# Performance work log

Hardware: AMD Instinct MI355X
Metric: run time of the kernel (lower is better)

## Reference

```python
import jax, jax.numpy as jnp
import numpy as np

FEATURE_DIM = 512


def setup_inputs() -> dict:
    key = jax.random.key(0)
    ks = jax.random.split(key, 12)
    B, Nv, Dv = 32, 1024, 768
    Nl, Dl = 77, 512
    D = FEATURE_DIM
    s = lambda fan_in: 1.0 / np.sqrt(fan_in)
    return {
        "fv": jax.random.normal(ks[0], (B, Nv, Dv), jnp.float32),
        "fl": jax.random.normal(ks[1], (B, Nl, Dl), jnp.float32),
        # linear_vk / linear_vv: Dv -> D (stored as [in, out])
        "W_vk": jax.random.uniform(ks[2], (Dv, D), jnp.float32, -s(Dv), s(Dv)),
        "b_vk": jax.random.uniform(ks[3], (D,), jnp.float32, -s(Dv), s(Dv)),
        "W_vv": jax.random.uniform(ks[4], (Dv, D), jnp.float32, -s(Dv), s(Dv)),
        "b_vv": jax.random.uniform(ks[5], (D,), jnp.float32, -s(Dv), s(Dv)),
        # linear_lk / linear_lv: Dl -> D
        "W_lk": jax.random.uniform(ks[6], (Dl, D), jnp.float32, -s(Dl), s(Dl)),
        "b_lk": jax.random.uniform(ks[7], (D,), jnp.float32, -s(Dl), s(Dl)),
        "W_lv": jax.random.uniform(ks[8], (Dl, D), jnp.float32, -s(Dl), s(Dl)),
        "b_lv": jax.random.uniform(ks[9], (D,), jnp.float32, -s(Dl), s(Dl)),
        # linear_m: nl(77) -> 768
        "W_m": jax.random.uniform(ks[10], (Nl, 768), jnp.float32, -s(Nl), s(Nl)),
        "b_m": jax.random.uniform(ks[11], (768,), jnp.float32, -s(Nl), s(Nl)),
    }


def reference(fv, fl, W_vk, b_vk, W_vv, b_vv, W_lk, b_lk, W_lv, b_lv, W_m, b_m):
    # projections
    fk_v = jnp.einsum("bvd,de->bve", fv, W_vk) + b_vk   # [B, Nv, D]
    fv_v = jnp.einsum("bvd,de->bve", fv, W_vv) + b_vv   # [B, Nv, D]
    fk_l = jnp.einsum("bld,de->ble", fl, W_lk) + b_lk   # [B, Nl, D]
    fv_l = jnp.einsum("bld,de->ble", fl, W_lv) + b_lv   # [B, Nl, D]
    # shared score matrix [B, Nl, Nv]
    a_raw = jnp.einsum("ble,bve->blv", fk_l, fk_v) / jnp.sqrt(
        jnp.asarray(FEATURE_DIM, fk_l.dtype))
    # dual softmax: over Nv for language queries, over Nl for vision queries
    fa_v = jnp.einsum("blv,bve->ble", jax.nn.softmax(a_raw, axis=-1), fv_v)  # [B, Nl, D]
    fa_l = jnp.einsum("bvl,ble->bve",
                      jax.nn.softmax(jnp.swapaxes(a_raw, -1, -2), axis=-1),
                      fv_l)                                                  # [B, Nv, D]
    # fm = fa_v @ fa_l^T -> [B, Nl, Nv]; transpose(1,2) -> [B, Nv, Nl]
    fm = jnp.einsum("bve,ble->bvl", fa_l, fa_v)          # [B, Nv, Nl]
    return jnp.einsum("bvl,lo->bvo", fm, W_m) + b_m      # [B, Nv, 768]
```

## Files before the change

kernel.cpp:

```cpp
#include <hip/hip_runtime.h>


using s16x8  = __attribute__((ext_vector_type(8))) short;
using f32x4v = __attribute__((ext_vector_type(4))) float;

__device__ __forceinline__ unsigned short f2bf(float f) {
  unsigned int u = __float_as_uint(f);
  u += 0x7fffu + ((u >> 16) & 1u);
  return (unsigned short)(u >> 16);
}
__device__ __forceinline__ float bf2f(unsigned short h) {
  return __uint_as_float(((unsigned int)h) << 16);
}
__device__ __forceinline__ void split2(float v, unsigned short &hh, unsigned short &ll) {
  hh = f2bf(v);
  ll = f2bf(v - bf2f(hh));
}
__device__ __forceinline__ void split8v(float4 a, float4 b, s16x8& H, s16x8& L) {
  unsigned short hh, ll;
  split2(a.x, hh, ll); H[0] = (short)hh; L[0] = (short)ll;
  split2(a.y, hh, ll); H[1] = (short)hh; L[1] = (short)ll;
  split2(a.z, hh, ll); H[2] = (short)hh; L[2] = (short)ll;
  split2(a.w, hh, ll); H[3] = (short)hh; L[3] = (short)ll;
  split2(b.x, hh, ll); H[4] = (short)hh; L[4] = (short)ll;
  split2(b.y, hh, ll); H[5] = (short)hh; L[5] = (short)ll;
  split2(b.z, hh, ll); H[6] = (short)hh; L[6] = (short)ll;
  split2(b.w, hh, ll); H[7] = (short)hh; L[7] = (short)ll;
}

__device__ __forceinline__ void gload16(const unsigned short* g, unsigned short* l) {
  __builtin_amdgcn_global_load_lds(
      (const __attribute__((address_space(1))) unsigned int*)(const void*)g,
      (__attribute__((address_space(3))) unsigned int*)(void*)l,
      16, 0, 0);
}

__global__ __launch_bounds__(256) void prep_weight(const float* __restrict__ W,
                                                   unsigned short* __restrict__ Wh,
                                                   unsigned short* __restrict__ Wl,
                                                   int K, int N, int Kpad) {
  __shared__ float tile[32][33];
  int nb = blockIdx.x * 32, kb = blockIdx.y * 32;
  int tx = threadIdx.x & 31, ty = threadIdx.x >> 5;
  #pragma unroll
  for (int i = 0; i < 32; i += 8) {
    int k = kb + ty + i, n = nb + tx;
    tile[ty + i][tx] = (k < K && n < N) ? W[(long)k * N + n] : 0.f;
  }
  __syncthreads();
  #pragma unroll
  for (int i = 0; i < 32; i += 8) {
    int n = nb + ty + i, k = kb + tx;
    if (n < N && k < Kpad) {
      unsigned short hh, ll;
      split2(tile[tx][ty + i], hh, ll);
      Wh[(long)n * Kpad + k] = hh;
      Wl[(long)n * Kpad + k] = ll;
    }
  }
}

struct GemmArgs {
  const unsigned short *Ah, *Alo, *Bh, *Blo;
  const float *Af;
  int K;
  int Mld, Nld;
  int lda, ldb;
  long long sA, sB;
};

template <bool AF32, bool SWZ, int NJ, class Epi>
__global__ __launch_bounds__(256, 4) void gemm3(GemmArgs g, Epi epi) {
  constexpr int BN  = NJ * 32;
  constexpr int ASZ = 128 * 32;
  constexpr int BSZ = BN * 32;
  __shared__ __align__(16) unsigned short sm[2 * ASZ + 2 * BSZ];
  unsigned short* sAh = sm;
  unsigned short* sAl = sm + ASZ;
  unsigned short* sBh = sm + 2 * ASZ;
  unsigned short* sBl = sm + 2 * ASZ + BSZ;

  int bidx = blockIdx.x, bidy = blockIdx.y;
  if constexpr (SWZ) {
    int nx = gridDim.x;
    int nwg = nx * gridDim.y;
    int orig = bidx + bidy * nx;
    int swz = (orig & 7) * (nwg >> 3) + (orig >> 3);
    bidx = swz % nx; bidy = swz / nx;
  }

  const int t    = threadIdx.x;
  const int b    = blockIdx.z;
  const int m0   = bidy * 128;
  const int n0   = bidx * BN;
  const int lane = t & 63;
  const int w    = t >> 6;
  const int wr   = (w >> 1) * 64;
  const int wc   = (w & 1) * (NJ * 16);

  const long long aBase = (long long)b * g.sA;
  const long long bBase = (long long)b * g.sB;

  const int clk = lane & 3;
  const int rwB = (NJ == 4) ? ((w << 5) + (lane >> 2)) : ((w << 4) + (lane >> 2));
  const int sckB = ((clk ^ ((rwB >> 1) & 3)) << 3);
  int br0 = n0 + rwB;      if (br0 > g.Nld - 1) br0 = g.Nld - 1;
  int br1 = n0 + rwB + 16; if (br1 > g.Nld - 1) br1 = g.Nld - 1;
  const long long bR0d = bBase + (long long)br0 * g.ldb + sckB;
  const long long bR1d = bBase + (long long)br1 * g.ldb + sckB;
  const int dB0 = (NJ == 4) ? (w << 10) : (w << 9);
  const int dB1 = dB0 + 512;
  const int rwA = (w << 5) + (lane >> 2);
  const int sckA = ((clk ^ ((rwA >> 1) & 3)) << 3);
  int arD0 = m0 + rwA;      if (arD0 > g.Mld - 1) arD0 = g.Mld - 1;
  int arD1 = m0 + rwA + 16; if (arD1 > g.Mld - 1) arD1 = g.Mld - 1;
  const long long aR0d = aBase + (long long)arD0 * g.lda + sckA;
  const long long aR1d = aBase + (long long)arD1 * g.lda + sckA;
  const int dA0 = w << 10, dA1 = (w << 10) + 512;

  const int rA0 = t >> 2, rA1 = 64 + (t >> 2), cc = t & 3;
  const int cOff = cc << 3;
  int mr0 = m0 + rA0; if (mr0 > g.Mld - 1) mr0 = g.Mld - 1;
  int mr1 = m0 + rA1; if (mr1 > g.Mld - 1) mr1 = g.Mld - 1;
  const long long aR0 = aBase + (long long)mr0 * g.lda;
  const long long aR1 = aBase + (long long)mr1 * g.lda;
  const int wA0 = rA0 * 32 + ((cc ^ ((rA0 >> 1) & 3)) << 3);
  const int wA1 = rA1 * 32 + ((cc ^ ((rA1 >> 1) & 3)) << 3);

  int roffA[4], roffB[NJ];
  #pragma unroll
  for (int i = 0; i < 4; ++i) {
    int row = wr + i * 16 + (lane & 15);
    int ch  = lane >> 4;
    roffA[i] = row * 32 + ((ch ^ ((row >> 1) & 3)) << 3);
  }
  #pragma unroll
  for (int j = 0; j < NJ; ++j) {
    int row = wc + j * 16 + (lane & 15);
    int ch  = lane >> 4;
    roffB[j] = row * 32 + ((ch ^ ((row >> 1) & 3)) << 3);
  }

  f32x4v acc[4][NJ];
  #pragma unroll
  for (int i = 0; i < 4; ++i)
    #pragma unroll
    for (int j = 0; j < NJ; ++j)
      #pragma unroll
      for (int r = 0; r < 4; ++r) acc[i][j][r] = 0.f;

  float4 pa0, pa1, pa2, pa3;

  auto issueDMA = [&](int k0) {
    gload16(g.Bh  + (bR0d + k0), sBh + dB0);
    gload16(g.Blo + (bR0d + k0), sBl + dB0);
    if constexpr (NJ == 4) {
      gload16(g.Bh  + (bR1d + k0), sBh + dB1);
      gload16(g.Blo + (bR1d + k0), sBl + dB1);
    }
    if constexpr (!AF32) {
      gload16(g.Ah  + (aR0d + k0), sAh + dA0);
      gload16(g.Ah  + (aR1d + k0), sAh + dA1);
      gload16(g.Alo + (aR0d + k0), sAl + dA0);
      gload16(g.Alo + (aR1d + k0), sAl + dA1);
    }
  };
  auto issueA = [&](int k0) {
    if constexpr (AF32) {
      const float* s0 = g.Af + (aR0 + k0 + cOff);
      const float* s1 = g.Af + (aR1 + k0 + cOff);
      pa0 = *(const float4*)s0; pa1 = *(const float4*)(s0 + 4);
      pa2 = *(const float4*)s1; pa3 = *(const float4*)(s1 + 4);
    }
  };
  auto writeA = [&]() {
    if constexpr (AF32) {
      s16x8 H, L;
      split8v(pa0, pa1, H, L);
      *(s16x8*)(sAh + wA0) = H; *(s16x8*)(sAl + wA0) = L;
      split8v(pa2, pa3, H, L);
      *(s16x8*)(sAh + wA1) = H; *(s16x8*)(sAl + wA1) = L;
    }
  };

  issueDMA(0);
  if constexpr (AF32) { issueA(0); writeA(); }
  const int nkt = g.K >> 5;
  for (int kt = 0; kt < nkt; ++kt) {
    asm volatile("s_waitcnt vmcnt(0)" ::: "memory");
    __syncthreads();
    if (AF32 && kt + 1 < nkt) issueA((kt + 1) << 5);
    s16x8 ah[4], al[4], bh[NJ], bl[NJ];
    #pragma unroll
    for (int i = 0; i < 4; ++i) {
      ah[i] = *(const s16x8*)(sAh + roffA[i]);
      al[i] = *(const s16x8*)(sAl + roffA[i]);
    }
    #pragma unroll
    for (int j = 0; j < NJ; ++j) {
      bh[j] = *(const s16x8*)(sBh + roffB[j]);
      bl[j] = *(const s16x8*)(sBl + roffB[j]);
    }
    #pragma unroll
    for (int i = 0; i < 4; ++i)
      #pragma unroll
      for (int j = 0; j < NJ; ++j) {
        acc[i][j] = __builtin_amdgcn_mfma_f32_16x16x32_bf16(ah[i], bh[j], acc[i][j], 0, 0, 0);
        acc[i][j] = __builtin_amdgcn_mfma_f32_16x16x32_bf16(ah[i], bl[j], acc[i][j], 0, 0, 0);
        acc[i][j] = __builtin_amdgcn_mfma_f32_16x16x32_bf16(al[i], bh[j], acc[i][j], 0, 0, 0);
      }
    __syncthreads();
    if (kt + 1 < nkt) {
      writeA();
      issueDMA((kt + 1) << 5);
    }
  }
  #pragma unroll
  for (int i = 0; i < 4; ++i)
    #pragma unroll
    for (int j = 0; j < NJ; ++j) {
      int mm = m0 + wr + i * 16 + ((lane >> 4) << 2);
      int nn = n0 + wc + j * 16 + (lane & 15);
      epi(b, mm, nn, acc[i][j]);
    }
}

struct EpiBF16Pair {
  unsigned short *h, *lo; const float* bias; long long bs; int ld; int Mst;
  __device__ void operator()(int b, int m, int n, f32x4v v) const {
    float bb = bias ? bias[n] : 0.f;
    #pragma unroll
    for (int r = 0; r < 4; ++r) {
      int mm = m + r;
      if (mm < Mst) {
        long long o = (long long)b * bs + (long long)mm * ld + n;
        unsigned short hh, ll;
        split2(v[r] + bb, hh, ll);
        h[o] = hh; lo[o] = ll;
      }
    }
  }
};

struct EpiDualL {
  unsigned short *kh, *kl, *vh, *vl; const float *bk, *bv;
  __device__ void operator()(int, int m, int n, f32x4v v) const {
    bool lo512 = n < 512;
    float bb = lo512 ? bk[n] : bv[n - 512];
    int nn = lo512 ? n : n - 512;
    unsigned short* H = lo512 ? kh : vh;
    unsigned short* L = lo512 ? kl : vl;
    #pragma unroll
    for (int r = 0; r < 4; ++r) {
      int mm = m + r;
      if (mm < 2464) {
        long long o = (long long)mm * 512 + nn;
        unsigned short hh, ll;
        split2(v[r] + bb, hh, ll);
        H[o] = hh; L[o] = ll;
      }
    }
  }
};

struct EpiDualV {
  unsigned short *kh, *kl, *vh, *vl; const float *bk, *bv;
  __device__ void operator()(int, int m, int n, f32x4v v) const {
    if (n < 512) {
      float bb = bk[n];
      #pragma unroll
      for (int r = 0; r < 4; ++r) {
        long long o = (long long)(m + r) * 512 + n;
        unsigned short hh, ll;
        split2(v[r] + bb, hh, ll);
        kh[o] = hh; kl[o] = ll;
      }
    } else {
      int b2 = m >> 10, vv = m & 1023;
      float bb = bv[n - 512];
      ushort4 H, L;
      split2(v[0] + bb, H.x, L.x); split2(v[1] + bb, H.y, L.y);
      split2(v[2] + bb, H.z, L.z); split2(v[3] + bb, H.w, L.w);
      long long o = ((long long)b2 * 512 + (n - 512)) * 1024 + vv;
      *(ushort4*)(vh + o) = H;
      *(ushort4*)(vl + o) = L;
    }
  }
};

struct EpiScore {
  float* out;
  __device__ void operator()(int b, int m, int n, f32x4v v) const {
    #pragma unroll
    for (int r = 0; r < 4; ++r) {
      int mm = m + r;
      if (mm < 77)
        out[((long long)b * 77 + mm) * 1024 + n] = v[r] * 0.04419417382415922f;
    }
  }
};

struct EpiTransT {
  unsigned short *h, *lo;
  __device__ void operator()(int b, int m, int n, f32x4v v) const {
    #pragma unroll
    for (int r = 0; r < 4; ++r) {
      int mm = m + r;
      float val = (mm < 77) ? v[r] : 0.f;
      long long o = (long long)b * 98304 + (long long)n * 128 + mm;
      unsigned short hh, ll;
      split2(val, hh, ll);
      h[o] = hh; lo[o] = ll;
    }
  }
};

struct EpiOutB {
  float* out; const float* bias;
  __device__ void operator()(int b, int m, int n, f32x4v v) const {
    float bb = bias[n];
    #pragma unroll
    for (int r = 0; r < 4; ++r)
      out[(long long)(b * 1024 + m + r) * 768 + n] = v[r] + bb;
  }
};

__global__ __launch_bounds__(256) void softmax_rows(const float* __restrict__ a,
                                                    unsigned short* __restrict__ Ph,
                                                    unsigned short* __restrict__ Plo) {
  long row = blockIdx.x;
  const float* src = a + row * 1024;
  int t = threadIdx.x;
  float4 x = ((const float4*)src)[t];
  float mx = fmaxf(fmaxf(x.x, x.y), fmaxf(x.z, x.w));
  #pragma unroll
  for (int o = 32; o; o >>= 1) mx = fmaxf(mx, __shfl_xor(mx, o));
  __shared__ float red[4], red2[4];
  int w = t >> 6;
  if ((t & 63) == 0) red[w] = mx;
  __syncthreads();
  mx = fmaxf(fmaxf(red[0], red[1]), fmaxf(red[2], red[3]));
  float e0 = __expf(x.x - mx), e1 = __expf(x.y - mx);
  float e2 = __expf(x.z - mx), e3 = __expf(x.w - mx);
  float s = e0 + e1 + e2 + e3;
  #pragma unroll
  for (int o = 32; o; o >>= 1) s += __shfl_xor(s, o);
  if ((t & 63) == 0) red2[w] = s;
  __syncthreads();
  s = red2[0] + red2[1] + red2[2] + red2[3];
  float inv = 1.f / s;
  ushort4 H, L;
  split2(e0 * inv, H.x, L.x); split2(e1 * inv, H.y, L.y);
  split2(e2 * inv, H.z, L.z); split2(e3 * inv, H.w, L.w);
  long o = row * 1024 + (long)t * 4;
  *(ushort4*)(Ph + o)  = H;
  *(ushort4*)(Plo + o) = L;
}

__global__ __launch_bounds__(128) void softmax_cols(const float* __restrict__ a,
                                                    unsigned short* __restrict__ Ph,
                                                    unsigned short* __restrict__ Plo) {
  __shared__ float tile[77 * 129];
  __shared__ float inv[128];
  int t = threadIdx.x;
  int c = blockIdx.x;
  int b = blockIdx.y;
  const float* src = a + (long)b * 77 * 1024 + c * 128;
  for (int r = 0; r < 77; ++r) tile[r * 129 + t] = src[(long)r * 1024 + t];
  __syncthreads();
  float mx = -1e30f;
  for (int r = 0; r < 77; ++r) mx = fmaxf(mx, tile[r * 129 + t]);
  float s = 0.f;
  for (int r = 0; r < 77; ++r) {
    float e = __expf(tile[r * 129 + t] - mx);
    tile[r * 129 + t] = e;
    s += e;
  }
  inv[t] = 1.f / s;
  __syncthreads();
  unsigned short* dh = Ph  + ((long)b * 1024 + c * 128) * 128;
  unsigned short* dl = Plo + ((long)b * 1024 + c * 128) * 128;
  for (int vb = 0; vb < 128; vb += 2) {
    int v = vb + (t >> 6);
    int k = (t & 63) * 2;
    float iv = inv[v];
    float p0 = (k     < 77) ? tile[k * 129 + v] * iv       : 0.f;
    float p1 = (k + 1 < 77) ? tile[(k + 1) * 129 + v] * iv : 0.f;
    ushort2 H, L;
    split2(p0, H.x, L.x); split2(p1, H.y, L.y);
    *(ushort2*)(dh + (long)v * 128 + k) = H;
    *(ushort2*)(dl + (long)v * 128 + k) = L;
  }
}

extern "C" void kernel_launch(void* const* d_in, const int* in_sizes, int n_in,
                              void* d_out, int out_size, void* d_ws, size_t ws_size,
                              hipStream_t stream) {
  const float* fv   = (const float*)d_in[0];
  const float* fl   = (const float*)d_in[1];
  const float* W_vk = (const float*)d_in[2];
  const float* b_vk = (const float*)d_in[3];
  const float* W_vv = (const float*)d_in[4];
  const float* b_vv = (const float*)d_in[5];
  const float* W_lk = (const float*)d_in[6];
  const float* b_lk = (const float*)d_in[7];
  const float* W_lv = (const float*)d_in[8];
  const float* b_lv = (const float*)d_in[9];
  const float* W_m  = (const float*)d_in[10];
  const float* b_m  = (const float*)d_in[11];

  char* base = (char*)d_ws;
  size_t off = 0;
  auto take = [&](size_t bytes) -> char* {
    char* p = base + off;
    off = (off + bytes + 255) & ~(size_t)255;
    return p;
  };

  unsigned short* wcatv_h = (unsigned short*)take(1572864);
  unsigned short* wcatv_l = (unsigned short*)take(1572864);
  unsigned short* wcatl_h = (unsigned short*)take(1048576);
  unsigned short* wcatl_l = (unsigned short*)take(1048576);
  unsigned short* wm_h    = (unsigned short*)take(196608);
  unsigned short* wm_l    = (unsigned short*)take(196608);
  unsigned short* fkl_h  = (unsigned short*)take(2523136);
  unsigned short* fkl_l  = (unsigned short*)take(2523136);
  unsigned short* fvl_h  = (unsigned short*)take(2523136);
  unsigned short* fvl_l  = (unsigned short*)take(2523136);
  unsigned short* fkv_h  = (unsigned short*)take(33554432);
  unsigned short* fkv_l  = (unsigned short*)take(33554432);
  unsigned short* fvvT_h = (unsigned short*)take(33554432);
  unsigned short* fvvT_l = (unsigned short*)take(33554432);
  float*          araw   = (float*)take(10092544);
  unsigned short* p1_h   = (unsigned short*)take(5046272);
  unsigned short* p1_l   = (unsigned short*)take(5046272);
  unsigned short* p2t_h  = (unsigned short*)take(8388608);
  unsigned short* p2t_l  = (unsigned short*)take(8388608);
  unsigned short* fav_h  = (unsigned short*)take(4194304);
  unsigned short* fav_l  = (unsigned short*)take(4194304);
  unsigned short* s_h    = (unsigned short*)take(1048576);
  unsigned short* s_l    = (unsigned short*)take(1048576);
  unsigned short* tt_h   = (unsigned short*)take(6291456);
  unsigned short* tt_l   = (unsigned short*)take(6291456);

  if (off > ws_size) return;

  prep_weight<<<dim3(16, 24), 256, 0, stream>>>(W_vk, wcatv_h, wcatv_l, 768, 512, 768);
  prep_weight<<<dim3(16, 24), 256, 0, stream>>>(W_vv, wcatv_h + 512 * 768, wcatv_l + 512 * 768, 768, 512, 768);
  prep_weight<<<dim3(16, 16), 256, 0, stream>>>(W_lk, wcatl_h, wcatl_l, 512, 512, 512);
  prep_weight<<<dim3(16, 16), 256, 0, stream>>>(W_lv, wcatl_h + 512 * 512, wcatl_l + 512 * 512, 512, 512, 512);
  prep_weight<<<dim3(24, 4), 256, 0, stream>>>(W_m, wm_h, wm_l, 77, 768, 128);

  {
    GemmArgs g{}; g.Af = fl; g.Bh = wcatl_h; g.Blo = wcatl_l;
    g.K = 512; g.Mld = 2464; g.Nld = 1024; g.lda = 512; g.ldb = 512; g.sA = 0; g.sB = 0;
    EpiDualL e{fkl_h, fkl_l, fvl_h, fvl_l, b_lk, b_lv};
    gemm3<true, false, 4, EpiDualL><<<dim3(8, 20, 1), 256, 0, stream>>>(g, e);
  }
  {
    GemmArgs g{}; g.Af = fv; g.Bh = wcatv_h; g.Blo = wcatv_l;
    g.K = 768; g.Mld = 32768; g.Nld = 1024; g.lda = 768; g.ldb = 768; g.sA = 0; g.sB = 0;
    EpiDualV e{fkv_h, fkv_l, fvvT_h, fvvT_l, b_vk, b_vv};
    gemm3<true, true, 4, EpiDualV><<<dim3(8, 256, 1), 256, 0, stream>>>(g, e);
  }
  {
    GemmArgs g{}; g.Ah = fkl_h; g.Alo = fkl_l; g.Bh = fkv_h; g.Blo = fkv_l;
    g.K = 512; g.Mld = 77; g.Nld = 1024; g.lda = 512; g.ldb = 512;
    g.sA = 77 * 512; g.sB = 1024 * 512;
    EpiScore e{araw};
    gemm3<false, false, 2, EpiScore><<<dim3(16, 1, 32), 256, 0, stream>>>(g, e);
  }
  softmax_rows<<<2464, 256, 0, stream>>>(araw, p1_h, p1_l);
  softmax_cols<<<dim3(8, 32), 128, 0, stream>>>(araw, p2t_h, p2t_l);
  {
    GemmArgs g{}; g.Ah = p1_h; g.Alo = p1_l; g.Bh = fvvT_h; g.Blo = fvvT_l;
    g.K = 1024; g.Mld = 77; g.Nld = 512; g.lda = 1024; g.ldb = 1024;
    g.sA = 77 * 1024; g.sB = 512 * 1024;
    EpiBF16Pair e{fav_h, fav_l, nullptr, 128 * 512, 512, 128};
    gemm3<false, false, 2, EpiBF16Pair><<<dim3(8, 1, 32), 256, 0, stream>>>(g, e);
  }
  {
    GemmArgs g{}; g.Ah = fvl_h; g.Alo = fvl_l; g.Bh = fav_h; g.Blo = fav_l;
    g.K = 512; g.Mld = 77; g.Nld = 128; g.lda = 512; g.ldb = 512;
    g.sA = 77 * 512; g.sB = 128 * 512;
    EpiBF16Pair e{s_h, s_l, nullptr, 128 * 128, 128, 128};
    gemm3<false, false, 2, EpiBF16Pair><<<dim3(2, 1, 32), 256, 0, stream>>>(g, e);
  }
  {
    GemmArgs g{}; g.Ah = s_h; g.Alo = s_l; g.Bh = wm_h; g.Blo = wm_l;
    g.K = 128; g.Mld = 128; g.Nld = 768; g.lda = 128; g.ldb = 128;
    g.sA = 128 * 128; g.sB = 0;
    EpiTransT e{tt_h, tt_l};
    gemm3<false, false, 2, EpiTransT><<<dim3(12, 1, 32), 256, 0, stream>>>(g, e);
  }
  {
    GemmArgs g{}; g.Ah = p2t_h; g.Alo = p2t_l; g.Bh = tt_h; g.Blo = tt_l;
    g.K = 128; g.Mld = 1024; g.Nld = 768; g.lda = 128; g.ldb = 128;
    g.sA = 1024 * 128; g.sB = 768 * 128;
    EpiOutB e{(float*)d_out, b_m};
    gemm3<false, false, 4, EpiOutB><<<dim3(6, 8, 32), 256, 0, stream>>>(g, e);
  }
  (void)in_sizes; (void)n_in; (void)out_size;
}
```

Baseline: 650.3 us.

## Double-buffer GEMM LDS tiles, add MI tile param, merge weight prep launches

Replaces the single-buffered GEMM with a ping-pong LDS pipeline. Loads for the next k-tile are issued into the alternate buffer before computing the current one, and the second barrier per iteration is removed. Adds an MI template parameter so the small batched GEMMs use 64-row tiles with twice as many blocks, and merges the five weight-prep launches into one kernel. The cost is doubled LDS per block, with launch bounds lowered to 2 blocks per CU, which may reduce occupancy.

```diff
diff --git a/kernel.cpp b/kernel.cpp
--- a/kernel.cpp
+++ b/kernel.cpp
@@ -35,27 +35,34 @@
       16, 0, 0);
 }
 
-__global__ __launch_bounds__(256) void prep_weight(const float* __restrict__ W,
-                                                   unsigned short* __restrict__ Wh,
-                                                   unsigned short* __restrict__ Wl,
-                                                   int K, int N, int Kpad) {
+struct PrepSeg { const float* W; unsigned short* Wh; unsigned short* Wl;
+                 int K, N, Kpad, ntx, tOff; };
+struct PrepArgs { PrepSeg s[5]; };
+
+__global__ __launch_bounds__(256) void prep_all(PrepArgs pa) {
   __shared__ float tile[32][33];
-  int nb = blockIdx.x * 32, kb = blockIdx.y * 32;
+  int bid = blockIdx.x;
+  int si = 0;
+  #pragma unroll
+  for (int i = 1; i < 5; ++i) if (bid >= pa.s[i].tOff) si = i;
+  PrepSeg sg = pa.s[si];
+  int local = bid - sg.tOff;
+  int nb = (local % sg.ntx) * 32, kb = (local / sg.ntx) * 32;
   int tx = threadIdx.x & 31, ty = threadIdx.x >> 5;
   #pragma unroll
   for (int i = 0; i < 32; i += 8) {
     int k = kb + ty + i, n = nb + tx;
-    tile[ty + i][tx] = (k < K && n < N) ? W[(long)k * N + n] : 0.f;
+    tile[ty + i][tx] = (k < sg.K && n < sg.N) ? sg.W[(long)k * sg.N + n] : 0.f;
   }
   __syncthreads();
   #pragma unroll
   for (int i = 0; i < 32; i += 8) {
     int n = nb + ty + i, k = kb + tx;
-    if (n < N && k < Kpad) {
+    if (n < sg.N && k < sg.Kpad) {
       unsigned short hh, ll;
       split2(tile[tx][ty + i], hh, ll);
-      Wh[(long)n * Kpad + k] = hh;
-      Wl[(long)n * Kpad + k] = ll;
+      sg.Wh[(long)n * sg.Kpad + k] = hh;
+      sg.Wl[(long)n * sg.Kpad + k] = ll;
     }
   }
 }
@@ -69,16 +76,13 @@
   long long sA, sB;
 };
 
-template <bool AF32, bool SWZ, int NJ, class Epi>
-__global__ __launch_bounds__(256, 4) void gemm3(GemmArgs g, Epi epi) {
-  constexpr int BN  = NJ * 32;
-  constexpr int ASZ = 128 * 32;
-  constexpr int BSZ = BN * 32;
-  __shared__ __align__(16) unsigned short sm[2 * ASZ + 2 * BSZ];
-  unsigned short* sAh = sm;
-  unsigned short* sAl = sm + ASZ;
-  unsigned short* sBh = sm + 2 * ASZ;
-  unsigned short* sBl = sm + 2 * ASZ + BSZ;
+template <bool AF32, bool SWZ, int MI, int NJ, class Epi>
+__global__ __launch_bounds__(256, 2) void gemmP(GemmArgs g, Epi epi) {
+  static_assert(!AF32 || MI == 4, "AF32 path assumes MI==4");
+  constexpr int ASZ = MI * 1024;
+  constexpr int BSZ = NJ * 1024;
+  constexpr int BUF = 2 * ASZ + 2 * BSZ;
+  __shared__ __align__(16) unsigned short sm[2 * BUF];
 
   int bidx = blockIdx.x, bidy = blockIdx.y;
   if constexpr (SWZ) {
@@ -91,11 +95,11 @@
 
   const int t    = threadIdx.x;
   const int b    = blockIdx.z;
-  const int m0   = bidy * 128;
-  const int n0   = bidx * BN;
+  const int m0   = bidy * (MI * 32);
+  const int n0   = bidx * (NJ * 32);
   const int lane = t & 63;
   const int w    = t >> 6;
-  const int wr   = (w >> 1) * 64;
+  const int wr   = (w >> 1) * (MI * 16);
   const int wc   = (w & 1) * (NJ * 16);
 
   const long long aBase = (long long)b * g.sA;
@@ -108,15 +112,16 @@
   int br1 = n0 + rwB + 16; if (br1 > g.Nld - 1) br1 = g.Nld - 1;
   const long long bR0d = bBase + (long long)br0 * g.ldb + sckB;
   const long long bR1d = bBase + (long long)br1 * g.ldb + sckB;
-  const int dB0 = (NJ == 4) ? (w << 10) : (w << 9);
+  const int dB0 = w * ((NJ == 4) ? 1024 : 512);
   const int dB1 = dB0 + 512;
-  const int rwA = (w << 5) + (lane >> 2);
+  const int rwA = (MI == 4) ? ((w << 5) + (lane >> 2)) : ((w << 4) + (lane >> 2));
   const int sckA = ((clk ^ ((rwA >> 1) & 3)) << 3);
   int arD0 = m0 + rwA;      if (arD0 > g.Mld - 1) arD0 = g.Mld - 1;
   int arD1 = m0 + rwA + 16; if (arD1 > g.Mld - 1) arD1 = g.Mld - 1;
   const long long aR0d = aBase + (long long)arD0 * g.lda + sckA;
   const long long aR1d = aBase + (long long)arD1 * g.lda + sckA;
-  const int dA0 = w << 10, dA1 = (w << 10) + 512;
+  const int dA0 = w * ((MI == 4) ? 1024 : 512);
+  const int dA1 = dA0 + 512;
 
   const int rA0 = t >> 2, rA1 = 64 + (t >> 2), cc = t & 3;
   const int cOff = cc << 3;
@@ -127,9 +132,9 @@
   const int wA0 = rA0 * 32 + ((cc ^ ((rA0 >> 1) & 3)) << 3);
   const int wA1 = rA1 * 32 + ((cc ^ ((rA1 >> 1) & 3)) << 3);
 
-  int roffA[4], roffB[NJ];
-  #pragma unroll
-  for (int i = 0; i < 4; ++i) {
+  int roffA[MI], roffB[NJ];
+  #pragma unroll
+  for (int i = 0; i < MI; ++i) {
     int row = wr + i * 16 + (lane & 15);
     int ch  = lane >> 4;
     roffA[i] = row * 32 + ((ch ^ ((row >> 1) & 3)) << 3);
@@ -141,9 +146,9 @@
     roffB[j] = row * 32 + ((ch ^ ((row >> 1) & 3)) << 3);
   }
 
-  f32x4v acc[4][NJ];
-  #pragma unroll
-  for (int i = 0; i < 4; ++i)
+  f32x4v acc[MI][NJ];
+  #pragma unroll
+  for (int i = 0; i < MI; ++i)
     #pragma unroll
     for (int j = 0; j < NJ; ++j)
       #pragma unroll
@@ -151,18 +156,21 @@
 
   float4 pa0, pa1, pa2, pa3;
 
-  auto issueDMA = [&](int k0) {
-    gload16(g.Bh  + (bR0d + k0), sBh + dB0);
-    gload16(g.Blo + (bR0d + k0), sBl + dB0);
+  auto issueDMA = [&](int k0, int p) {
+    unsigned short* bb = sm + p * BUF;
+    gload16(g.Bh  + (bR0d + k0), bb + 2 * ASZ + dB0);
+    gload16(g.Blo + (bR0d + k0), bb + 2 * ASZ + BSZ + dB0);
     if constexpr (NJ == 4) {
-      gload16(g.Bh  + (bR1d + k0), sBh + dB1);
-      gload16(g.Blo + (bR1d + k0), sBl + dB1);
+      gload16(g.Bh  + (bR1d + k0), bb + 2 * ASZ + dB1);
+      gload16(g.Blo + (bR1d + k0), bb + 2 * ASZ + BSZ + dB1);
     }
     if constexpr (!AF32) {
-      gload16(g.Ah  + (aR0d + k0), sAh + dA0);
-      gload16(g.Ah  + (aR1d + k0), sAh + dA1);
-      gload16(g.Alo + (aR0d + k0), sAl + dA0);
-      gload16(g.Alo + (aR1d + k0), sAl + dA1);
+      gload16(g.Ah  + (aR0d + k0), bb + dA0);
+      gload16(g.Alo + (aR0d + k0), bb + ASZ + dA0);
+      if constexpr (MI == 4) {
+        gload16(g.Ah  + (aR1d + k0), bb + dA1);
+        gload16(g.Alo + (aR1d + k0), bb + ASZ + dA1);
+      }
     }
   };
   auto issueA = [&](int k0) {
@@ -173,50 +181,53 @@
       pa2 = *(const float4*)s1; pa3 = *(const float4*)(s1 + 4);
     }
   };
-  auto writeA = [&]() {
+  auto writeA = [&](int p) {
     if constexpr (AF32) {
+      unsigned short* base = sm + p * BUF;
       s16x8 H, L;
       split8v(pa0, pa1, H, L);
-      *(s16x8*)(sAh + wA0) = H; *(s16x8*)(sAl + wA0) = L;
+      *(s16x8*)(base + wA0) = H; *(s16x8*)(base + ASZ + wA0) = L;
       split8v(pa2, pa3, H, L);
-      *(s16x8*)(sAh + wA1) = H; *(s16x8*)(sAl + wA1) = L;
+      *(s16x8*)(base + wA1) = H; *(s16x8*)(base + ASZ + wA1) = L;
     }
   };
 
-  issueDMA(0);
-  if constexpr (AF32) { issueA(0); writeA(); }
+  issueDMA(0, 0);
+  if constexpr (AF32) { issueA(0); writeA(0); }
+  int p = 0;
   const int nkt = g.K >> 5;
   for (int kt = 0; kt < nkt; ++kt) {
     asm volatile("s_waitcnt vmcnt(0)" ::: "memory");
     __syncthreads();
-    if (AF32 && kt + 1 < nkt) issueA((kt + 1) << 5);
-    s16x8 ah[4], al[4], bh[NJ], bl[NJ];
-    #pragma unroll
-    for (int i = 0; i < 4; ++i) {
-      ah[i] = *(const s16x8*)(sAh + roffA[i]);
-      al[i] = *(const s16x8*)(sAl + roffA[i]);
+    if (kt + 1 < nkt) {
+      issueDMA((kt + 1) << 5, p ^ 1);
+      issueA((kt + 1) << 5);
+    }
+    unsigned short* base = sm + p * BUF;
+    s16x8 ah[MI], al[MI], bh[NJ], bl[NJ];
+    #pragma unroll
+    for (int i = 0; i < MI; ++i) {
+      ah[i] = *(const s16x8*)(base + roffA[i]);
+      al[i] = *(const s16x8*)(base + ASZ + roffA[i]);
     }
     #pragma unroll
     for (int j = 0; j < NJ; ++j) {
-      bh[j] = *(const s16x8*)(sBh + roffB[j]);
-      bl[j] = *(const s16x8*)(sBl + roffB[j]);
-    }
-    #pragma unroll
-    for (int i = 0; i < 4; ++i)
+      bh[j] = *(const s16x8*)(base + 2 * ASZ + roffB[j]);
+      bl[j] = *(const s16x8*)(base + 2 * ASZ + BSZ + roffB[j]);
+    }
+    #pragma unroll
+    for (int i = 0; i < MI; ++i)
       #pragma unroll
       for (int j = 0; j < NJ; ++j) {
         acc[i][j] = __builtin_amdgcn_mfma_f32_16x16x32_bf16(ah[i], bh[j], acc[i][j], 0, 0, 0);
         acc[i][j] = __builtin_amdgcn_mfma_f32_16x16x32_bf16(ah[i], bl[j], acc[i][j], 0, 0, 0);
         acc[i][j] = __builtin_amdgcn_mfma_f32_16x16x32_bf16(al[i], bh[j], acc[i][j], 0, 0, 0);
       }
-    __syncthreads();
-    if (kt + 1 < nkt) {
-      writeA();
-      issueDMA((kt + 1) << 5);
-    }
-  }
-  #pragma unroll
-  for (int i = 0; i < 4; ++i)
+    if (kt + 1 < nkt) writeA(p ^ 1);
+    p ^= 1;
+  }
+  #pragma unroll
+  for (int i = 0; i < MI; ++i)
     #pragma unroll
     for (int j = 0; j < NJ; ++j) {
       int mm = m0 + wr + i * 16 + ((lane >> 4) << 2);
@@ -445,30 +456,34 @@
 
   if (off > ws_size) return;
 
-  prep_weight<<<dim3(16, 24), 256, 0, stream>>>(W_vk, wcatv_h, wcatv_l, 768, 512, 768);
-  prep_weight<<<dim3(16, 24), 256, 0, stream>>>(W_vv, wcatv_h + 512 * 768, wcatv_l + 512 * 768, 768, 512, 768);
-  prep_weight<<<dim3(16, 16), 256, 0, stream>>>(W_lk, wcatl_h, wcatl_l, 512, 512, 512);
-  prep_weight<<<dim3(16, 16), 256, 0, stream>>>(W_lv, wcatl_h + 512 * 512, wcatl_l + 512 * 512, 512, 512, 512);
-  prep_weight<<<dim3(24, 4), 256, 0, stream>>>(W_m, wm_h, wm_l, 77, 768, 128);
+  {
+    PrepArgs pa;
+    pa.s[0] = {W_vk, wcatv_h,               wcatv_l,               768, 512, 768, 16, 0};
+    pa.s[1] = {W_vv, wcatv_h + 512 * 768,   wcatv_l + 512 * 768,   768, 512, 768, 16, 384};
+    pa.s[2] = {W_lk, wcatl_h,               wcatl_l,               512, 512, 512, 16, 768};
+    pa.s[3] = {W_lv, wcatl_h + 512 * 512,   wcatl_l + 512 * 512,   512, 512, 512, 16, 1024};
+    pa.s[4] = {W_m,  wm_h,                  wm_l,                   77, 768, 128, 24, 1280};
+    prep_all<<<1376, 256, 0, stream>>>(pa);
+  }
 
   {
     GemmArgs g{}; g.Af = fl; g.Bh = wcatl_h; g.Blo = wcatl_l;
     g.K = 512; g.Mld = 2464; g.Nld = 1024; g.lda = 512; g.ldb = 512; g.sA = 0; g.sB = 0;
     EpiDualL e{fkl_h, fkl_l, fvl_h, fvl_l, b_lk, b_lv};
-    gemm3<true, false, 4, EpiDualL><<<dim3(8, 20, 1), 256, 0, stream>>>(g, e);
+    gemmP<true, false, 4, 4, EpiDualL><<<dim3(8, 20, 1), 256, 0, stream>>>(g, e);
   }
   {
     GemmArgs g{}; g.Af = fv; g.Bh = wcatv_h; g.Blo = wcatv_l;
     g.K = 768; g.Mld = 32768; g.Nld = 1024; g.lda = 768; g.ldb = 768; g.sA = 0; g.sB = 0;
     EpiDualV e{fkv_h, fkv_l, fvvT_h, fvvT_l, b_vk, b_vv};
-    gemm3<true, true, 4, EpiDualV><<<dim3(8, 256, 1), 256, 0, stream>>>(g, e);
+    gemmP<true, true, 4, 4, EpiDualV><<<dim3(8, 256, 1), 256, 0, stream>>>(g, e);
   }
   {
     GemmArgs g{}; g.Ah = fkl_h; g.Alo = fkl_l; g.Bh = fkv_h; g.Blo = fkv_l;
     g.K = 512; g.Mld = 77; g.Nld = 1024; g.lda = 512; g.ldb = 512;
     g.sA = 77 * 512; g.sB = 1024 * 512;
     EpiScore e{araw};
-    gemm3<false, false, 2, EpiScore><<<dim3(16, 1, 32), 256, 0, stream>>>(g, e);
+    gemmP<false, false, 2, 2, EpiScore><<<dim3(16, 2, 32), 256, 0, stream>>>(g, e);
   }
   softmax_rows<<<2464, 256, 0, stream>>>(araw, p1_h, p1_l);
   softmax_cols<<<dim3(8, 32), 128, 0, stream>>>(araw, p2t_h, p2t_l);
@@ -477,28 +492,28 @@
     g.K = 1024; g.Mld = 77; g.Nld = 512; g.lda = 1024; g.ldb = 1024;
     g.sA = 77 * 1024; g.sB = 512 * 1024;
     EpiBF16Pair e{fav_h, fav_l, nullptr, 128 * 512, 512, 128};
-    gemm3<false, false, 2, EpiBF16Pair><<<dim3(8, 1, 32), 256, 0, stream>>>(g, e);
+    gemmP<false, false, 2, 2, EpiBF16Pair><<<dim3(8, 2, 32), 256, 0, stream>>>(g, e);
   }
   {
     GemmArgs g{}; g.Ah = fvl_h; g.Alo = fvl_l; g.Bh = fav_h; g.Blo = fav_l;
     g.K = 512; g.Mld = 77; g.Nld = 128; g.lda = 512; g.ldb = 512;
     g.sA = 77 * 512; g.sB = 128 * 512;
     EpiBF16Pair e{s_h, s_l, nullptr, 128 * 128, 128, 128};
-    gemm3<false, false, 2, EpiBF16Pair><<<dim3(2, 1, 32), 256, 0, stream>>>(g, e);
+    gemmP<false, false, 2, 2, EpiBF16Pair><<<dim3(2, 2, 32), 256, 0, stream>>>(g, e);
   }
   {
     GemmArgs g{}; g.Ah = s_h; g.Alo = s_l; g.Bh = wm_h; g.Blo = wm_l;
     g.K = 128; g.Mld = 128; g.Nld = 768; g.lda = 128; g.ldb = 128;
     g.sA = 128 * 128; g.sB = 0;
     EpiTransT e{tt_h, tt_l};
-    gemm3<false, false, 2, EpiTransT><<<dim3(12, 1, 32), 256, 0, stream>>>(g, e);
+    gemmP<false, false, 2, 2, EpiTransT><<<dim3(12, 2, 32), 256, 0, stream>>>(g, e);
   }
   {
     GemmArgs g{}; g.Ah = p2t_h; g.Alo = p2t_l; g.Bh = tt_h; g.Blo = tt_l;
     g.K = 128; g.Mld = 1024; g.Nld = 768; g.lda = 128; g.ldb = 128;
     g.sA = 1024 * 128; g.sB = 768 * 128;
     EpiOutB e{(float*)d_out, b_m};
-    gemm3<false, false, 4, EpiOutB><<<dim3(6, 8, 32), 256, 0, stream>>>(g, e);
+    gemmP<false, false, 4, 4, EpiOutB><<<dim3(6, 8, 32), 256, 0, stream>>>(g, e);
   }
   (void)in_sizes; (void)n_in; (void)out_size;
 }
```

Result: faster. 548.1 us (-15.7%).
